# Optimization experiments

Measured on AMD Instinct MI355X. Metric: run time of the kernel, lower is better.

The kernel has to match this reference:

```python
import jax, jax.numpy as jnp
import numpy as np
from jax.ops import segment_sum

IN_DIM, HID_DIM, OUT_DIM = 128, 128, 64
N_NODES, N_EDGES = 50000, 800000


def gcn_conv(x, src, dst, W, b, n_nodes):
    # Symmetric GCN normalization (no self loops): deg at targets from unit weights
    deg = segment_sum(jnp.ones(src.shape[0], dtype=x.dtype), dst, num_segments=n_nodes)
    dinv = jnp.where(deg > 0, jax.lax.rsqrt(jnp.maximum(deg, 1.0)), 0.0)
    norm = dinv[src] * dinv[dst]                      # [E]
    h = x @ W                                         # [N, out] small GEMM first (PyG order)
    msg = h[src] * norm[:, None]                      # gather + scale: [E, out]
    out = segment_sum(msg, dst, num_segments=n_nodes) # scatter-add to targets
    return out + b


def setup_inputs() -> dict:
    key = jax.random.key(0)
    k1, k2, k3, k4, k5 = jax.random.split(key, 5)
    x = jax.random.normal(k1, (N_NODES, IN_DIM), dtype=jnp.float32)
    edge_index = jax.random.randint(k2, (2, N_EDGES), 0, N_NODES, dtype=jnp.int64)
    s1 = 1.0 / np.sqrt(IN_DIM)
    s2 = 1.0 / np.sqrt(HID_DIM)
    W1 = jax.random.uniform(k3, (IN_DIM, HID_DIM), jnp.float32, -s1, s1)
    b1 = jnp.zeros((HID_DIM,), jnp.float32)
    W2 = jax.random.uniform(k4, (HID_DIM, OUT_DIM), jnp.float32, -s2, s2)
    b2 = jnp.zeros((OUT_DIM,), jnp.float32)
    return {"x": x, "edge_index": edge_index, "W1": W1, "b1": b1, "W2": W2, "b2": b2}


def reference(x, edge_index, W1, b1, W2, b2):
    n_nodes = x.shape[0]
    src, dst = edge_index[0], edge_index[1]
    h = gcn_conv(x, src, dst, W1, b1, n_nodes)
    h = jax.nn.relu(h)
    # Dropout is identity in eval mode (reference is deterministic)
    out = gcn_conv(h, src, dst, W2, b2, n_nodes)
    return out
```

## Files before the change

### kernel.cpp

```cpp
#include <hip/hip_runtime.h>

#define N_NODES 50000
#define N_EDGES 800000
#define IN_DIM  128
#define HID_DIM 128
#define OUT_DIM 64

#define NPAD 50176
#define NB 7
#define KEYS (N_NODES * NB)
#define KPAD 350208
#define NB_SCAN2 (KPAD / 1024)
#define FILLB ((N_EDGES / 4 + 255) / 256)
#define GEMM1B ((N_NODES + 63) / 64)
#define DINVB ((N_NODES + 1023) / 1024)

typedef __attribute__((ext_vector_type(8))) short bf16x8;
typedef __attribute__((ext_vector_type(4))) float f32x4;

__device__ __forceinline__ unsigned short f2bf(float f) {
    unsigned u = __float_as_uint(f);
    u += 0x7fffu + ((u >> 16) & 1u);
    return (unsigned short)(u >> 16);
}
__device__ __forceinline__ float bflo(unsigned u) { return __uint_as_float(u << 16); }
__device__ __forceinline__ float bfhi(unsigned u) { return __uint_as_float(u & 0xffff0000u); }

#define ACC8(u)  do { \
    acc[0] += bflo(u.x); acc[1] += bfhi(u.x); \
    acc[2] += bflo(u.y); acc[3] += bfhi(u.y); \
    acc[4] += bflo(u.z); acc[5] += bfhi(u.z); \
    acc[6] += bflo(u.w); acc[7] += bfhi(u.w); } while (0)


__global__ void rank_hist_kernel(const int* __restrict__ src, const int* __restrict__ dst,
                                 int* __restrict__ cnt2, int* __restrict__ rank) {
    int e = (blockIdx.x * 256 + threadIdx.x) * 4;
    if (e >= N_EDGES) return;
    int4 s4 = *(const int4*)(src + e);
    int4 d4 = *(const int4*)(dst + e);
    int k0 = d4.x * NB + (s4.x >> 13);
    int k1 = d4.y * NB + (s4.y >> 13);
    int k2 = d4.z * NB + (s4.z >> 13);
    int k3 = d4.w * NB + (s4.w >> 13);
    int r0 = atomicAdd(&cnt2[k0], 1);
    int r1 = atomicAdd(&cnt2[k1], 1);
    int r2 = atomicAdd(&cnt2[k2], 1);
    int r3 = atomicAdd(&cnt2[k3], 1);
    *(int4*)(rank + e) = make_int4(r0, r1, r2, r3);
}


__global__ __launch_bounds__(1024) void prep_kernel(const int* __restrict__ cnt2,
                                                    int* __restrict__ blockSums,
                                                    float* __restrict__ dinv,
                                                    const float* __restrict__ W1,
                                                    const float* __restrict__ W2,
                                                    unsigned short* __restrict__ w1t,
                                                    unsigned short* __restrict__ w2t) {
    int bid = blockIdx.x;
    if (bid < NB_SCAN2) {
        __shared__ int s[1024];
        int i = bid * 1024 + threadIdx.x;
        s[threadIdx.x] = (i < KEYS) ? cnt2[i] : 0;
        __syncthreads();
        for (int off = 512; off > 0; off >>= 1) {
            if (threadIdx.x < off) s[threadIdx.x] += s[threadIdx.x + off];
            __syncthreads();
        }
        if (threadIdx.x == 0) blockSums[bid] = s[0];
    } else if (bid < NB_SCAN2 + DINVB) {
        int d = (bid - NB_SCAN2) * 1024 + threadIdx.x;
        if (d < N_NODES) {
            int base = d * NB;
            int deg = cnt2[base] + cnt2[base + 1] + cnt2[base + 2] + cnt2[base + 3]
                    + cnt2[base + 4] + cnt2[base + 5] + cnt2[base + 6];
            dinv[d] = (deg > 0) ? rsqrtf((float)deg) : 0.0f;
        }
    } else if (bid < NB_SCAN2 + DINVB + 4) {
        int idx = (bid - NB_SCAN2 - DINVB) * 1024 + threadIdx.x;
        int c = idx >> 5, k4 = (idx & 31) * 4;
        ushort4 o;
        o.x = f2bf(W1[(k4 + 0) * 128 + c]);
        o.y = f2bf(W1[(k4 + 1) * 128 + c]);
        o.z = f2bf(W1[(k4 + 2) * 128 + c]);
        o.w = f2bf(W1[(k4 + 3) * 128 + c]);
        *(ushort4*)(w1t + c * 128 + k4) = o;
    } else {
        int idx = (bid - NB_SCAN2 - DINVB - 4) * 1024 + threadIdx.x;
        if (idx >= 64 * 32) return;
        int c = idx >> 5, k4 = (idx & 31) * 4;
        ushort4 o;
        o.x = f2bf(W2[(k4 + 0) * 64 + c]);
        o.y = f2bf(W2[(k4 + 1) * 64 + c]);
        o.z = f2bf(W2[(k4 + 2) * 64 + c]);
        o.w = f2bf(W2[(k4 + 3) * 64 + c]);
        *(ushort4*)(w2t + c * 128 + k4) = o;
    }
}


__global__ __launch_bounds__(1024) void scan_kernel(const int* __restrict__ cnt2,
                                                    const int* __restrict__ blockSums,
                                                    int* __restrict__ rs) {
    __shared__ int s[1024];
    __shared__ int sums[NB_SCAN2];
    __shared__ int base_s;
    if (threadIdx.x < NB_SCAN2) sums[threadIdx.x] = blockSums[threadIdx.x];
    if (blockIdx.x == 0 && threadIdx.x == 0) rs[KEYS] = N_EDGES;
    int i = blockIdx.x * 1024 + threadIdx.x;
    int v = (i < KEYS) ? cnt2[i] : 0;
    s[threadIdx.x] = v;
    __syncthreads();
    if (threadIdx.x == 0) {
        int run = 0;
        for (int b = 0; b < (int)blockIdx.x; ++b) run += sums[b];
        base_s = run;
    }
    for (int off = 1; off < 1024; off <<= 1) {
        int t = (threadIdx.x >= off) ? s[threadIdx.x - off] : 0;
        __syncthreads();
        s[threadIdx.x] += t;
        __syncthreads();
    }
    if (i < KEYS) rs[i] = base_s + s[threadIdx.x] - v;
}


__global__ __launch_bounds__(256) void fill_gemm1_kernel(const int* __restrict__ src,
                                                         const int* __restrict__ dst,
                                                         const int* __restrict__ rank,
                                                         const int* __restrict__ rs,
                                                         int* __restrict__ csr_src,
                                                         const float* __restrict__ x,
                                                         const unsigned short* __restrict__ w1t,
                                                         const float* __restrict__ dinv,
                                                         unsigned short* __restrict__ h1b) {
    int bid = blockIdx.x;
    if (bid < FILLB) {
        int e = (bid * 256 + threadIdx.x) * 4;
        if (e >= N_EDGES) return;
        int4 s4 = *(const int4*)(src + e);
        int4 d4 = *(const int4*)(dst + e);
        int4 r4 = *(const int4*)(rank + e);
        csr_src[rs[d4.x * NB + (s4.x >> 13)] + r4.x] = s4.x;
        csr_src[rs[d4.y * NB + (s4.y >> 13)] + r4.y] = s4.y;
        csr_src[rs[d4.z * NB + (s4.z >> 13)] + r4.z] = s4.z;
        csr_src[rs[d4.w * NB + (s4.w >> 13)] + r4.w] = s4.w;
        return;
    }

    int gb = bid - FILLB;
    int wave = threadIdx.x >> 6;
    int lane = threadIdx.x & 63;
    int n = lane & 15, quad = lane >> 4;
    int row0 = gb * 64 + wave * 16;

    int arow = row0 + n;
    if (arow >= N_NODES) arow = N_NODES - 1;
    const float* aptr = x + (size_t)arow * 128 + quad * 8;
    const unsigned short* bbase = w1t + (size_t)n * 128 + quad * 8;

    f32x4 acc[8];
#pragma unroll
    for (int t = 0; t < 8; ++t) acc[t] = (f32x4){0.f, 0.f, 0.f, 0.f};

#pragma unroll
    for (int w4 = 0; w4 < 4; ++w4) {
        float4 f0 = *(const float4*)(aptr + w4 * 32);
        float4 f1 = *(const float4*)(aptr + w4 * 32 + 4);
        bf16x8 af;
        af[0] = (short)f2bf(f0.x); af[1] = (short)f2bf(f0.y);
        af[2] = (short)f2bf(f0.z); af[3] = (short)f2bf(f0.w);
        af[4] = (short)f2bf(f1.x); af[5] = (short)f2bf(f1.y);
        af[6] = (short)f2bf(f1.z); af[7] = (short)f2bf(f1.w);
#pragma unroll
        for (int t = 0; t < 8; ++t) {
            bf16x8 bf = *(const bf16x8*)(bbase + (size_t)t * 2048 + w4 * 32);
            acc[t] = __builtin_amdgcn_mfma_f32_16x16x32_bf16(af, bf, acc[t], 0, 0, 0);
        }
    }

#pragma unroll
    for (int r = 0; r < 4; ++r) {
        int row = row0 + quad * 4 + r;
        if (row < N_NODES) {
            float dn = dinv[row];
            unsigned short* o = h1b + (size_t)row * 128 + n;
#pragma unroll
            for (int t = 0; t < 8; ++t) o[t * 16] = f2bf(acc[t][r] * dn);
        }
    }
}


#define A1T_STRIDE 136

__global__ __launch_bounds__(256) void agg1_gemm2_fused(const int* __restrict__ csr_src,
                                                        const int* __restrict__ rs,
                                                        const float* __restrict__ dinv,
                                                        const float* __restrict__ b1,
                                                        const unsigned short* __restrict__ h1b,
                                                        const unsigned short* __restrict__ w2t,
                                                        unsigned short* __restrict__ h2b) {
    __shared__ unsigned short a1t[16 * A1T_STRIDE];

    int node0 = blockIdx.x * 16;
    int g = threadIdx.x >> 4;
    int q = threadIdx.x & 15;
    int node = node0 + g;
    int start = rs[node * NB];
    int m = rs[node * NB + NB] - start;

    float acc[8] = {};
    int j = 0;
    for (; j + 3 < m; j += 4) {
        int s0 = csr_src[start + j];
        int s1 = csr_src[start + j + 1];
        int s2 = csr_src[start + j + 2];
        int s3 = csr_src[start + j + 3];
        uint4 u0 = ((const uint4*)(h1b + (size_t)s0 * 128))[q];
        uint4 u1 = ((const uint4*)(h1b + (size_t)s1 * 128))[q];
        uint4 u2 = ((const uint4*)(h1b + (size_t)s2 * 128))[q];
        uint4 u3 = ((const uint4*)(h1b + (size_t)s3 * 128))[q];
        ACC8(u0); ACC8(u1); ACC8(u2); ACC8(u3);
    }
    for (; j < m; ++j) {
        int s0 = csr_src[start + j];
        uint4 u0 = ((const uint4*)(h1b + (size_t)s0 * 128))[q];
        ACC8(u0);
    }

    {
        float dn = dinv[node];
        float4 bA = ((const float4*)b1)[2 * q];
        float4 bB = ((const float4*)b1)[2 * q + 1];
        ushort4 oA, oB;
        oA.x = f2bf(fmaxf(acc[0] * dn + bA.x, 0.f));
        oA.y = f2bf(fmaxf(acc[1] * dn + bA.y, 0.f));
        oA.z = f2bf(fmaxf(acc[2] * dn + bA.z, 0.f));
        oA.w = f2bf(fmaxf(acc[3] * dn + bA.w, 0.f));
        oB.x = f2bf(fmaxf(acc[4] * dn + bB.x, 0.f));
        oB.y = f2bf(fmaxf(acc[5] * dn + bB.y, 0.f));
        oB.z = f2bf(fmaxf(acc[6] * dn + bB.z, 0.f));
        oB.w = f2bf(fmaxf(acc[7] * dn + bB.w, 0.f));
        ushort4* o = (ushort4*)(a1t + g * A1T_STRIDE + q * 8);
        o[0] = oA;
        o[1] = oB;
    }
    __syncthreads();

    int wave = threadIdx.x >> 6;
    int lane = threadIdx.x & 63;
    int n = lane & 15, quad = lane >> 4;
    const unsigned short* bbase = w2t + (size_t)(wave * 16 + n) * 128 + quad * 8;
    const unsigned short* abase = a1t + (size_t)n * A1T_STRIDE + quad * 8;

    f32x4 c2 = (f32x4){0.f, 0.f, 0.f, 0.f};
#pragma unroll
    for (int w4 = 0; w4 < 4; ++w4) {
        bf16x8 af = *(const bf16x8*)(abase + w4 * 32);
        bf16x8 bf = *(const bf16x8*)(bbase + w4 * 32);
        c2 = __builtin_amdgcn_mfma_f32_16x16x32_bf16(af, bf, c2, 0, 0, 0);
    }

#pragma unroll
    for (int r = 0; r < 4; ++r) {
        int row = node0 + quad * 4 + r;
        float dn = dinv[row];
        h2b[(size_t)row * 64 + wave * 16 + n] = f2bf(c2[r] * dn);
    }
}


__global__ __launch_bounds__(256) void agg2_kernel(const int* __restrict__ csr_src,
                                                   const int* __restrict__ rs,
                                                   const float* __restrict__ dinv,
                                                   const float* __restrict__ b2,
                                                   const unsigned short* __restrict__ h2b,
                                                   float* __restrict__ out) {
    int node = blockIdx.x * 4 + (threadIdx.x >> 6);
    if (node >= N_NODES) return;
    int lane = threadIdx.x & 63;
    int grp = lane >> 3;
    int q   = lane & 7;
    int start = rs[node * NB];
    int m = rs[node * NB + NB] - start;

    float acc[8] = {};

    int j = grp;
    for (; j + 8 < m; j += 16) {
        int s0 = csr_src[start + j];
        int s1 = csr_src[start + j + 8];
        uint4 u0 = ((const uint4*)(h2b + (size_t)s0 * 64))[q];
        uint4 u1 = ((const uint4*)(h2b + (size_t)s1 * 64))[q];
        ACC8(u0); ACC8(u1);
    }
    if (j < m) {
        int s0 = csr_src[start + j];
        uint4 u0 = ((const uint4*)(h2b + (size_t)s0 * 64))[q];
        ACC8(u0);
    }

#pragma unroll
    for (int d = 8; d <= 32; d <<= 1) {
#pragma unroll
        for (int c = 0; c < 8; ++c) acc[c] += __shfl_xor(acc[c], d, 64);
    }

    if (lane < 8) {
        float dn = dinv[node];
        float4 bA = ((const float4*)b2)[2 * q];
        float4 bB = ((const float4*)b2)[2 * q + 1];
        float4 rA, rB;
        rA.x = acc[0] * dn + bA.x;
        rA.y = acc[1] * dn + bA.y;
        rA.z = acc[2] * dn + bA.z;
        rA.w = acc[3] * dn + bA.w;
        rB.x = acc[4] * dn + bB.x;
        rB.y = acc[5] * dn + bB.y;
        rB.z = acc[6] * dn + bB.z;
        rB.w = acc[7] * dn + bB.w;
        float4* o = (float4*)(out + (size_t)node * 64);
        o[2 * q] = rA;
        o[2 * q + 1] = rB;
    }
}


extern "C" void kernel_launch(void* const* d_in, const int* in_sizes, int n_in,
                              void* d_out, int out_size, void* d_ws, size_t ws_size,
                              hipStream_t stream) {
    const float* x  = (const float*)d_in[0];
    const int*   ei = (const int*)d_in[1];
    const float* W1 = (const float*)d_in[2];
    const float* b1 = (const float*)d_in[3];
    const float* W2 = (const float*)d_in[4];
    const float* b2 = (const float*)d_in[5];
    float* out = (float*)d_out;

    const int* src = ei;
    const int* dst = ei + N_EDGES;

    char* ws = (char*)d_ws;
    int*   cnt2      = (int*)ws;
    int*   rs        = cnt2 + KPAD;
    int*   blockSums = rs + KPAD;
    float* dinv      = (float*)(blockSums + 384);
    int*   rank      = (int*)(dinv + NPAD);
    int*   csr_src   = rank + N_EDGES;
    unsigned short* h1b = (unsigned short*)(csr_src + N_EDGES);
    unsigned short* h2b = h1b + (size_t)N_NODES * HID_DIM;
    unsigned short* w1t = h2b + (size_t)N_NODES * OUT_DIM;
    unsigned short* w2t = w1t + 128 * 128;

    hipMemsetAsync(cnt2, 0, KPAD * sizeof(int), stream);

    rank_hist_kernel<<<(N_EDGES / 4 + 255) / 256, 256, 0, stream>>>(src, dst, cnt2, rank);

    prep_kernel<<<NB_SCAN2 + DINVB + 6, 1024, 0, stream>>>(cnt2, blockSums, dinv,
                                                           W1, W2, w1t, w2t);

    scan_kernel<<<NB_SCAN2, 1024, 0, stream>>>(cnt2, blockSums, rs);

    fill_gemm1_kernel<<<FILLB + GEMM1B, 256, 0, stream>>>(src, dst, rank, rs, csr_src,
                                                          x, w1t, dinv, h1b);

    agg1_gemm2_fused<<<N_NODES / 16, 256, 0, stream>>>(csr_src, rs, dinv, b1, h1b, w2t, h2b);

    agg2_kernel<<<(N_NODES + 3) / 4, 256, 0, stream>>>(csr_src, rs, dinv, b2, h2b, out);
}
```

Measured before the change: 208.8 us.

## Overlap GEMM1 with histogram and store source dinv alongside CSR indices

Moves the first GEMM so it runs in the same launch as the edge histogram, overlapping compute with atomic-bound work. The per-source dinv scaling is moved from the GEMM1 epilogue into the CSR entries, which are now int2 pairs carrying the dinv value, and layer-1 aggregation applies it with an FMA per edge. The memset and weight transpose are merged into one init kernel. In exchange the fill kernel becomes standalone, CSR traffic doubles (8 bytes per edge, also read by agg2), and there is one extra kernel launch.

```diff
diff --git a/kernel.cpp b/kernel.cpp
--- a/kernel.cpp
+++ b/kernel.cpp
@@ -11,8 +11,10 @@
 #define KEYS (N_NODES * NB)
 #define KPAD 350208
 #define NB_SCAN2 (KPAD / 1024)
+#define ZEROB (KPAD / 1024)
+#define HISTB ((N_EDGES / 4 + 255) / 256)
+#define GEMM1B ((N_NODES + 63) / 64)
 #define FILLB ((N_EDGES / 4 + 255) / 256)
-#define GEMM1B ((N_NODES + 63) / 64)
 #define DINVB ((N_NODES + 1023) / 1024)
 
 typedef __attribute__((ext_vector_type(8))) short bf16x8;
@@ -25,6 +27,12 @@
 }
 __device__ __forceinline__ float bflo(unsigned u) { return __uint_as_float(u << 16); }
 __device__ __forceinline__ float bfhi(unsigned u) { return __uint_as_float(u & 0xffff0000u); }
+
+#define ACC8N(u, nrm)  do { \
+    acc[0] = fmaf(nrm, bflo(u.x), acc[0]); acc[1] = fmaf(nrm, bfhi(u.x), acc[1]); \
+    acc[2] = fmaf(nrm, bflo(u.y), acc[2]); acc[3] = fmaf(nrm, bfhi(u.y), acc[3]); \
+    acc[4] = fmaf(nrm, bflo(u.z), acc[4]); acc[5] = fmaf(nrm, bfhi(u.z), acc[5]); \
+    acc[6] = fmaf(nrm, bflo(u.w), acc[6]); acc[7] = fmaf(nrm, bfhi(u.w), acc[7]); } while (0)
 
 #define ACC8(u)  do { \
     acc[0] += bflo(u.x); acc[1] += bfhi(u.x); \
@@ -33,31 +41,106 @@
     acc[6] += bflo(u.w); acc[7] += bfhi(u.w); } while (0)
 
 
-__global__ void rank_hist_kernel(const int* __restrict__ src, const int* __restrict__ dst,
-                                 int* __restrict__ cnt2, int* __restrict__ rank) {
-    int e = (blockIdx.x * 256 + threadIdx.x) * 4;
-    if (e >= N_EDGES) return;
-    int4 s4 = *(const int4*)(src + e);
-    int4 d4 = *(const int4*)(dst + e);
-    int k0 = d4.x * NB + (s4.x >> 13);
-    int k1 = d4.y * NB + (s4.y >> 13);
-    int k2 = d4.z * NB + (s4.z >> 13);
-    int k3 = d4.w * NB + (s4.w >> 13);
-    int r0 = atomicAdd(&cnt2[k0], 1);
-    int r1 = atomicAdd(&cnt2[k1], 1);
-    int r2 = atomicAdd(&cnt2[k2], 1);
-    int r3 = atomicAdd(&cnt2[k3], 1);
-    *(int4*)(rank + e) = make_int4(r0, r1, r2, r3);
-}
-
-
-__global__ __launch_bounds__(1024) void prep_kernel(const int* __restrict__ cnt2,
-                                                    int* __restrict__ blockSums,
-                                                    float* __restrict__ dinv,
-                                                    const float* __restrict__ W1,
-                                                    const float* __restrict__ W2,
-                                                    unsigned short* __restrict__ w1t,
-                                                    unsigned short* __restrict__ w2t) {
+__global__ void init_kernel(int* __restrict__ cnt2,
+                            const float* __restrict__ W1, const float* __restrict__ W2,
+                            unsigned short* __restrict__ w1t, unsigned short* __restrict__ w2t) {
+    int bid = blockIdx.x;
+    if (bid < ZEROB) {
+        int i = (bid * 256 + threadIdx.x) * 4;
+        *(int4*)(cnt2 + i) = make_int4(0, 0, 0, 0);
+    } else if (bid < ZEROB + 16) {
+        int idx = (bid - ZEROB) * 256 + threadIdx.x;
+        int c = idx >> 5, k4 = (idx & 31) * 4;
+        ushort4 o;
+        o.x = f2bf(W1[(k4 + 0) * 128 + c]);
+        o.y = f2bf(W1[(k4 + 1) * 128 + c]);
+        o.z = f2bf(W1[(k4 + 2) * 128 + c]);
+        o.w = f2bf(W1[(k4 + 3) * 128 + c]);
+        *(ushort4*)(w1t + c * 128 + k4) = o;
+    } else {
+        int idx = (bid - ZEROB - 16) * 256 + threadIdx.x;
+        int c = idx >> 5, k4 = (idx & 31) * 4;
+        ushort4 o;
+        o.x = f2bf(W2[(k4 + 0) * 64 + c]);
+        o.y = f2bf(W2[(k4 + 1) * 64 + c]);
+        o.z = f2bf(W2[(k4 + 2) * 64 + c]);
+        o.w = f2bf(W2[(k4 + 3) * 64 + c]);
+        *(ushort4*)(w2t + c * 128 + k4) = o;
+    }
+}
+
+
+__global__ __launch_bounds__(256) void hist_gemm1_kernel(const int* __restrict__ src,
+                                                         const int* __restrict__ dst,
+                                                         int* __restrict__ cnt2,
+                                                         int* __restrict__ rank,
+                                                         const float* __restrict__ x,
+                                                         const unsigned short* __restrict__ w1t,
+                                                         unsigned short* __restrict__ h1b) {
+    int bid = blockIdx.x;
+    if (bid < HISTB) {
+        int e = (bid * 256 + threadIdx.x) * 4;
+        if (e >= N_EDGES) return;
+        int4 s4 = *(const int4*)(src + e);
+        int4 d4 = *(const int4*)(dst + e);
+        int k0 = d4.x * NB + (s4.x >> 13);
+        int k1 = d4.y * NB + (s4.y >> 13);
+        int k2 = d4.z * NB + (s4.z >> 13);
+        int k3 = d4.w * NB + (s4.w >> 13);
+        int r0 = atomicAdd(&cnt2[k0], 1);
+        int r1 = atomicAdd(&cnt2[k1], 1);
+        int r2 = atomicAdd(&cnt2[k2], 1);
+        int r3 = atomicAdd(&cnt2[k3], 1);
+        *(int4*)(rank + e) = make_int4(r0, r1, r2, r3);
+        return;
+    }
+
+    int gb = bid - HISTB;
+    int wave = threadIdx.x >> 6;
+    int lane = threadIdx.x & 63;
+    int n = lane & 15, quad = lane >> 4;
+    int row0 = gb * 64 + wave * 16;
+
+    int arow = row0 + n;
+    if (arow >= N_NODES) arow = N_NODES - 1;
+    const float* aptr = x + (size_t)arow * 128 + quad * 8;
+    const unsigned short* bbase = w1t + (size_t)n * 128 + quad * 8;
+
+    f32x4 acc[8];
+#pragma unroll
+    for (int t = 0; t < 8; ++t) acc[t] = (f32x4){0.f, 0.f, 0.f, 0.f};
+
+#pragma unroll
+    for (int w4 = 0; w4 < 4; ++w4) {
+        float4 f0 = *(const float4*)(aptr + w4 * 32);
+        float4 f1 = *(const float4*)(aptr + w4 * 32 + 4);
+        bf16x8 af;
+        af[0] = (short)f2bf(f0.x); af[1] = (short)f2bf(f0.y);
+        af[2] = (short)f2bf(f0.z); af[3] = (short)f2bf(f0.w);
+        af[4] = (short)f2bf(f1.x); af[5] = (short)f2bf(f1.y);
+        af[6] = (short)f2bf(f1.z); af[7] = (short)f2bf(f1.w);
+#pragma unroll
+        for (int t = 0; t < 8; ++t) {
+            bf16x8 bf = *(const bf16x8*)(bbase + (size_t)t * 2048 + w4 * 32);
+            acc[t] = __builtin_amdgcn_mfma_f32_16x16x32_bf16(af, bf, acc[t], 0, 0, 0);
+        }
+    }
+
+#pragma unroll
+    for (int r = 0; r < 4; ++r) {
+        int row = row0 + quad * 4 + r;
+        if (row < N_NODES) {
+            unsigned short* o = h1b + (size_t)row * 128 + n;
+#pragma unroll
+            for (int t = 0; t < 8; ++t) o[t * 16] = f2bf(acc[t][r]);
+        }
+    }
+}
+
+
+__global__ __launch_bounds__(1024) void reduce_dinv_kernel(const int* __restrict__ cnt2,
+                                                           int* __restrict__ blockSums,
+                                                           float* __restrict__ dinv) {
     int bid = blockIdx.x;
     if (bid < NB_SCAN2) {
         __shared__ int s[1024];
@@ -69,7 +152,7 @@
             __syncthreads();
         }
         if (threadIdx.x == 0) blockSums[bid] = s[0];
-    } else if (bid < NB_SCAN2 + DINVB) {
+    } else {
         int d = (bid - NB_SCAN2) * 1024 + threadIdx.x;
         if (d < N_NODES) {
             int base = d * NB;
@@ -77,25 +160,6 @@
                     + cnt2[base + 4] + cnt2[base + 5] + cnt2[base + 6];
             dinv[d] = (deg > 0) ? rsqrtf((float)deg) : 0.0f;
         }
-    } else if (bid < NB_SCAN2 + DINVB + 4) {
-        int idx = (bid - NB_SCAN2 - DINVB) * 1024 + threadIdx.x;
-        int c = idx >> 5, k4 = (idx & 31) * 4;
-        ushort4 o;
-        o.x = f2bf(W1[(k4 + 0) * 128 + c]);
-        o.y = f2bf(W1[(k4 + 1) * 128 + c]);
-        o.z = f2bf(W1[(k4 + 2) * 128 + c]);
-        o.w = f2bf(W1[(k4 + 3) * 128 + c]);
-        *(ushort4*)(w1t + c * 128 + k4) = o;
-    } else {
-        int idx = (bid - NB_SCAN2 - DINVB - 4) * 1024 + threadIdx.x;
-        if (idx >= 64 * 32) return;
-        int c = idx >> 5, k4 = (idx & 31) * 4;
-        ushort4 o;
-        o.x = f2bf(W2[(k4 + 0) * 64 + c]);
-        o.y = f2bf(W2[(k4 + 1) * 64 + c]);
-        o.z = f2bf(W2[(k4 + 2) * 64 + c]);
-        o.w = f2bf(W2[(k4 + 3) * 64 + c]);
-        *(ushort4*)(w2t + c * 128 + k4) = o;
     }
 }
 
@@ -127,76 +191,24 @@
 }
 
 
-__global__ __launch_bounds__(256) void fill_gemm1_kernel(const int* __restrict__ src,
-                                                         const int* __restrict__ dst,
-                                                         const int* __restrict__ rank,
-                                                         const int* __restrict__ rs,
-                                                         int* __restrict__ csr_src,
-                                                         const float* __restrict__ x,
-                                                         const unsigned short* __restrict__ w1t,
-                                                         const float* __restrict__ dinv,
-                                                         unsigned short* __restrict__ h1b) {
-    int bid = blockIdx.x;
-    if (bid < FILLB) {
-        int e = (bid * 256 + threadIdx.x) * 4;
-        if (e >= N_EDGES) return;
-        int4 s4 = *(const int4*)(src + e);
-        int4 d4 = *(const int4*)(dst + e);
-        int4 r4 = *(const int4*)(rank + e);
-        csr_src[rs[d4.x * NB + (s4.x >> 13)] + r4.x] = s4.x;
-        csr_src[rs[d4.y * NB + (s4.y >> 13)] + r4.y] = s4.y;
-        csr_src[rs[d4.z * NB + (s4.z >> 13)] + r4.z] = s4.z;
-        csr_src[rs[d4.w * NB + (s4.w >> 13)] + r4.w] = s4.w;
-        return;
-    }
-
-    int gb = bid - FILLB;
-    int wave = threadIdx.x >> 6;
-    int lane = threadIdx.x & 63;
-    int n = lane & 15, quad = lane >> 4;
-    int row0 = gb * 64 + wave * 16;
-
-    int arow = row0 + n;
-    if (arow >= N_NODES) arow = N_NODES - 1;
-    const float* aptr = x + (size_t)arow * 128 + quad * 8;
-    const unsigned short* bbase = w1t + (size_t)n * 128 + quad * 8;
-
-    f32x4 acc[8];
-#pragma unroll
-    for (int t = 0; t < 8; ++t) acc[t] = (f32x4){0.f, 0.f, 0.f, 0.f};
-
-#pragma unroll
-    for (int w4 = 0; w4 < 4; ++w4) {
-        float4 f0 = *(const float4*)(aptr + w4 * 32);
-        float4 f1 = *(const float4*)(aptr + w4 * 32 + 4);
-        bf16x8 af;
-        af[0] = (short)f2bf(f0.x); af[1] = (short)f2bf(f0.y);
-        af[2] = (short)f2bf(f0.z); af[3] = (short)f2bf(f0.w);
-        af[4] = (short)f2bf(f1.x); af[5] = (short)f2bf(f1.y);
-        af[6] = (short)f2bf(f1.z); af[7] = (short)f2bf(f1.w);
-#pragma unroll
-        for (int t = 0; t < 8; ++t) {
-            bf16x8 bf = *(const bf16x8*)(bbase + (size_t)t * 2048 + w4 * 32);
-            acc[t] = __builtin_amdgcn_mfma_f32_16x16x32_bf16(af, bf, acc[t], 0, 0, 0);
-        }
-    }
-
-#pragma unroll
-    for (int r = 0; r < 4; ++r) {
-        int row = row0 + quad * 4 + r;
-        if (row < N_NODES) {
-            float dn = dinv[row];
-            unsigned short* o = h1b + (size_t)row * 128 + n;
-#pragma unroll
-            for (int t = 0; t < 8; ++t) o[t * 16] = f2bf(acc[t][r] * dn);
-        }
-    }
+__global__ void fill_kernel(const int* __restrict__ src, const int* __restrict__ dst,
+                            const int* __restrict__ rank, const int* __restrict__ rs,
+                            const float* __restrict__ dinv, int2* __restrict__ csr2) {
+    int e = (blockIdx.x * 256 + threadIdx.x) * 4;
+    if (e >= N_EDGES) return;
+    int4 s4 = *(const int4*)(src + e);
+    int4 d4 = *(const int4*)(dst + e);
+    int4 r4 = *(const int4*)(rank + e);
+    csr2[rs[d4.x * NB + (s4.x >> 13)] + r4.x] = make_int2(s4.x, __float_as_int(dinv[s4.x]));
+    csr2[rs[d4.y * NB + (s4.y >> 13)] + r4.y] = make_int2(s4.y, __float_as_int(dinv[s4.y]));
+    csr2[rs[d4.z * NB + (s4.z >> 13)] + r4.z] = make_int2(s4.z, __float_as_int(dinv[s4.z]));
+    csr2[rs[d4.w * NB + (s4.w >> 13)] + r4.w] = make_int2(s4.w, __float_as_int(dinv[s4.w]));
 }
 
 
 #define A1T_STRIDE 136
 
-__global__ __launch_bounds__(256) void agg1_gemm2_fused(const int* __restrict__ csr_src,
+__global__ __launch_bounds__(256) void agg1_gemm2_fused(const int2* __restrict__ csr2,
                                                         const int* __restrict__ rs,
                                                         const float* __restrict__ dinv,
                                                         const float* __restrict__ b1,
@@ -215,20 +227,23 @@
     float acc[8] = {};
     int j = 0;
     for (; j + 3 < m; j += 4) {
-        int s0 = csr_src[start + j];
-        int s1 = csr_src[start + j + 1];
-        int s2 = csr_src[start + j + 2];
-        int s3 = csr_src[start + j + 3];
-        uint4 u0 = ((const uint4*)(h1b + (size_t)s0 * 128))[q];
-        uint4 u1 = ((const uint4*)(h1b + (size_t)s1 * 128))[q];
-        uint4 u2 = ((const uint4*)(h1b + (size_t)s2 * 128))[q];
-        uint4 u3 = ((const uint4*)(h1b + (size_t)s3 * 128))[q];
-        ACC8(u0); ACC8(u1); ACC8(u2); ACC8(u3);
+        int2 p0 = csr2[start + j];
+        int2 p1 = csr2[start + j + 1];
+        int2 p2 = csr2[start + j + 2];
+        int2 p3 = csr2[start + j + 3];
+        uint4 u0 = ((const uint4*)(h1b + (size_t)p0.x * 128))[q];
+        uint4 u1 = ((const uint4*)(h1b + (size_t)p1.x * 128))[q];
+        uint4 u2 = ((const uint4*)(h1b + (size_t)p2.x * 128))[q];
+        uint4 u3 = ((const uint4*)(h1b + (size_t)p3.x * 128))[q];
+        float n0 = __int_as_float(p0.y), n1 = __int_as_float(p1.y);
+        float n2 = __int_as_float(p2.y), n3 = __int_as_float(p3.y);
+        ACC8N(u0, n0); ACC8N(u1, n1); ACC8N(u2, n2); ACC8N(u3, n3);
     }
     for (; j < m; ++j) {
-        int s0 = csr_src[start + j];
-        uint4 u0 = ((const uint4*)(h1b + (size_t)s0 * 128))[q];
-        ACC8(u0);
+        int2 p0 = csr2[start + j];
+        uint4 u0 = ((const uint4*)(h1b + (size_t)p0.x * 128))[q];
+        float n0 = __int_as_float(p0.y);
+        ACC8N(u0, n0);
     }
 
     {
@@ -273,7 +288,7 @@
 }
 
 
-__global__ __launch_bounds__(256) void agg2_kernel(const int* __restrict__ csr_src,
+__global__ __launch_bounds__(256) void agg2_kernel(const int2* __restrict__ csr2,
                                                    const int* __restrict__ rs,
                                                    const float* __restrict__ dinv,
                                                    const float* __restrict__ b2,
@@ -291,14 +306,14 @@
 
     int j = grp;
     for (; j + 8 < m; j += 16) {
-        int s0 = csr_src[start + j];
-        int s1 = csr_src[start + j + 8];
+        int s0 = csr2[start + j].x;
+        int s1 = csr2[start + j + 8].x;
         uint4 u0 = ((const uint4*)(h2b + (size_t)s0 * 64))[q];
         uint4 u1 = ((const uint4*)(h2b + (size_t)s1 * 64))[q];
         ACC8(u0); ACC8(u1);
     }
     if (j < m) {
-        int s0 = csr_src[start + j];
+        int s0 = csr2[start + j].x;
         uint4 u0 = ((const uint4*)(h2b + (size_t)s0 * 64))[q];
         ACC8(u0);
     }
@@ -349,25 +364,23 @@
     int*   blockSums = rs + KPAD;
     float* dinv      = (float*)(blockSums + 384);
     int*   rank      = (int*)(dinv + NPAD);
-    int*   csr_src   = rank + N_EDGES;
-    unsigned short* h1b = (unsigned short*)(csr_src + N_EDGES);
+    int2*  csr2      = (int2*)(rank + N_EDGES);
+    unsigned short* h1b = (unsigned short*)(csr2 + N_EDGES);
     unsigned short* h2b = h1b + (size_t)N_NODES * HID_DIM;
     unsigned short* w1t = h2b + (size_t)N_NODES * OUT_DIM;
     unsigned short* w2t = w1t + 128 * 128;
 
-    hipMemsetAsync(cnt2, 0, KPAD * sizeof(int), stream);
-
-    rank_hist_kernel<<<(N_EDGES / 4 + 255) / 256, 256, 0, stream>>>(src, dst, cnt2, rank);
-
-    prep_kernel<<<NB_SCAN2 + DINVB + 6, 1024, 0, stream>>>(cnt2, blockSums, dinv,
-                                                           W1, W2, w1t, w2t);
+    init_kernel<<<ZEROB + 24, 256, 0, stream>>>(cnt2, W1, W2, w1t, w2t);
+
+    hist_gemm1_kernel<<<HISTB + GEMM1B, 256, 0, stream>>>(src, dst, cnt2, rank, x, w1t, h1b);
+
+    reduce_dinv_kernel<<<NB_SCAN2 + DINVB, 1024, 0, stream>>>(cnt2, blockSums, dinv);
 
     scan_kernel<<<NB_SCAN2, 1024, 0, stream>>>(cnt2, blockSums, rs);
 
-    fill_gemm1_kernel<<<FILLB + GEMM1B, 256, 0, stream>>>(src, dst, rank, rs, csr_src,
-                                                          x, w1t, dinv, h1b);
-
-    agg1_gemm2_fused<<<N_NODES / 16, 256, 0, stream>>>(csr_src, rs, dinv, b1, h1b, w2t, h2b);
-
-    agg2_kernel<<<(N_NODES + 3) / 4, 256, 0, stream>>>(csr_src, rs, dinv, b2, h2b, out);
-}
+    fill_kernel<<<FILLB, 256, 0, stream>>>(src, dst, rank, rs, dinv, csr2);
+
+    agg1_gemm2_fused<<<N_NODES / 16, 256, 0, stream>>>(csr2, rs, dinv, b1, h1b, w2t, h2b);
+
+    agg2_kernel<<<(N_NODES + 3) / 4, 256, 0, stream>>>(csr2, rs, dinv, b2, h2b, out);
+}
```

Measured after the change: 210.4 us. No clear change (+0.7%).
